# Kernel tuning notes

Measured on AMD Instinct MI355X. Metric: run time of the kernel, lower is better.

Reference implementation:

```python
import jax, jax.numpy as jnp
import numpy as np

B = 4096
D1 = 2048   # APPEARANCE_DIM
D2 = 1024   # POSE_DIM
DF = 8192   # FUSED_DIM
LN_EPS = 1e-5
L2_EPS = 1e-12


def setup_inputs() -> dict:
    key = jax.random.key(0)
    ks = jax.random.split(key, 6)
    x = jax.random.normal(ks[0], (B, D1), dtype=jnp.float32)
    y = jax.random.normal(ks[1], (B, D2), dtype=jnp.float32)
    h1 = jax.random.randint(ks[2], (D1,), 0, DF, dtype=jnp.int32)
    h2 = jax.random.randint(ks[3], (D2,), 0, DF, dtype=jnp.int32)
    s1 = (2 * jax.random.randint(ks[4], (D1,), 0, 2) - 1).astype(jnp.float32)
    s2 = (2 * jax.random.randint(ks[5], (D2,), 0, 2) - 1).astype(jnp.float32)
    gamma = jnp.ones((DF,), dtype=jnp.float32)
    beta = jnp.zeros((DF,), dtype=jnp.float32)
    return {"x": x, "y": y, "s1": s1, "s2": s2, "gamma": gamma,
            "beta": beta, "h1": h1, "h2": h2}


def count_sketch(v, h, s, out_dim):
    # v: [B, Din], h: [Din] int indices into out_dim, s: [Din] +-1 signs
    # single vectorized scatter-add along the feature axis
    return jnp.zeros((v.shape[0], out_dim), v.dtype).at[:, h].add(v * s)


def reference(x, y, s1, s2, gamma, beta, h1, h2):
    x_sk = count_sketch(x, h1, s1, DF)          # [B, DF]
    y_sk = count_sketch(y, h2, s2, DF)          # [B, DF]
    # circular convolution via FFT
    fused = jnp.fft.ifft(jnp.fft.fft(x_sk, axis=1) * jnp.fft.fft(y_sk, axis=1),
                         axis=1).real           # [B, DF]
    # LayerNorm over last dim
    mu = jnp.mean(fused, axis=-1, keepdims=True)
    var = jnp.mean(jnp.square(fused - mu), axis=-1, keepdims=True)
    normed = (fused - mu) * jax.lax.rsqrt(var + LN_EPS) * gamma + beta
    # F.normalize(p=2, dim=1)
    nrm = jnp.linalg.norm(normed, axis=1, keepdims=True)
    return normed / jnp.maximum(nrm, L2_EPS)
```

## Files before the change

### kernel.cpp

```cpp
#include <hip/hip_runtime.h>
#include <math.h>

#define DF 8192
#define NT 1024

#define SW(i) ((i) ^ ((((i) >> 4) & 7) << 2))

__device__ __forceinline__ float2 cmul(float2 a, float2 b) {
    return make_float2(a.x * b.x - a.y * b.y, a.x * b.y + a.y * b.x);
}
__device__ __forceinline__ float2 cadd(float2 a, float2 b) { return make_float2(a.x + b.x, a.y + b.y); }
__device__ __forceinline__ float2 csub(float2 a, float2 b) { return make_float2(a.x - b.x, a.y - b.y); }
__device__ __forceinline__ float2 cmuli(float2 a)  { return make_float2(-a.y, a.x); }
__device__ __forceinline__ float2 cmulmi(float2 a) { return make_float2(a.y, -a.x); }

#define RT_H 0.70710678118654752f

__device__ __forceinline__ int brev10(int x) { return (int)(__brev((unsigned)x) >> 22); }

__device__ __forceinline__ void bf_dif(float2& a, float2& b, float2 W) {
    float2 d = csub(a, b);
    a = cadd(a, b);
    b = cmul(d, W);
}
__device__ __forceinline__ void bf_dit(float2& a, float2& b, float2 W) {
    float2 bw = cmul(b, W);
    float2 ta = a;
    a = cadd(ta, bw);
    b = csub(ta, bw);
}
__device__ __forceinline__ void bf_dit1(float2& a, float2& b) {
    float2 tb = b, ta = a;
    a = cadd(ta, tb);
    b = csub(ta, tb);
}
__device__ __forceinline__ void bf_diti(float2& a, float2& b) {
    float2 bw = cmuli(b);
    float2 ta = a;
    a = cadd(ta, bw);
    b = csub(ta, bw);
}

__device__ __forceinline__ void fft8_dif(float2 v[8], float2 w) {
    const float2 w2 = cmul(w, w);
    const float2 w4 = cmul(w2, w2);
    bf_dif(v[0], v[4], w);
    bf_dif(v[1], v[5], cmul(w, make_float2(RT_H, -RT_H)));
    bf_dif(v[2], v[6], cmulmi(w));
    bf_dif(v[3], v[7], cmul(w, make_float2(-RT_H, -RT_H)));
    bf_dif(v[0], v[2], w2);
    bf_dif(v[1], v[3], cmulmi(w2));
    bf_dif(v[4], v[6], w2);
    bf_dif(v[5], v[7], cmulmi(w2));
    bf_dif(v[0], v[1], w4);
    bf_dif(v[2], v[3], w4);
    bf_dif(v[4], v[5], w4);
    bf_dif(v[6], v[7], w4);
}

__device__ __forceinline__ void fft4_dit(float2 v[4], float2 q) {
    const float2 q2 = cmul(q, q);
    bf_dit(v[0], v[1], q2);
    bf_dit(v[2], v[3], q2);
    bf_dit(v[0], v[2], q);
    bf_dit(v[1], v[3], cmuli(q));
}

__device__ __forceinline__ float2 mega_combine(float2 A, float2 B, float2 PA, float2 PB,
                                               float2 W, float invN) {
    float X1r = 0.5f * (A.x + PB.x), X1i = 0.5f * (A.y - PB.y);
    float Y1r = 0.5f * (A.y + PB.y), Y1i = 0.5f * (PB.x - A.x);
    float2 P1 = make_float2((X1r * Y1r - X1i * Y1i) * invN, (X1r * Y1i + X1i * Y1r) * invN);
    float X2r = 0.5f * (B.x + PA.x), X2i = 0.5f * (B.y - PA.y);
    float Y2r = 0.5f * (B.y + PA.y), Y2i = 0.5f * (PA.x - B.x);
    float2 P2 = make_float2((X2r * Y2r - X2i * Y2i) * invN, (X2r * Y2i + X2i * Y2r) * invN);
    float2 S = cadd(P1, P2);
    float2 D = csub(P1, P2);
    float2 Dw = cmul(D, W);
    return make_float2(S.x - Dw.y, S.y + Dw.x);
}

__global__ __launch_bounds__(NT, 8)
void mcb5(const float* __restrict__ x, const float* __restrict__ y,
          const float* __restrict__ s1, const float* __restrict__ s2,
          const float* __restrict__ gamma, const float* __restrict__ beta,
          const int* __restrict__ h1, const int* __restrict__ h2,
          float* __restrict__ out)
{
    __shared__ float2 z[DF];
    const int t = threadIdx.x;
    const int row = blockIdx.x;

    {
        float4* z4 = (float4*)z;
        #pragma unroll
        for (int m = 0; m < 4; ++m) z4[t + NT * m] = make_float4(0.f, 0.f, 0.f, 0.f);
    }
    __syncthreads();

    {
        float2 xv = ((const float2*)(x + (size_t)row * 2048))[t];
        float2 sv = ((const float2*)s1)[t];
        int2   hv = ((const int2*)h1)[t];
        atomicAdd(&z[SW(hv.x)].x, xv.x * sv.x);
        atomicAdd(&z[SW(hv.y)].x, xv.y * sv.y);
        float yv = (y + (size_t)row * 1024)[t];
        atomicAdd(&z[SW(h2[t])].y, yv * s2[t]);
    }
    __syncthreads();

    float sn, cs;

    {
        float2 v[8];
        #pragma unroll
        for (int m = 0; m < 8; ++m) v[m] = z[SW(t + 1024 * m)];
        __sincosf(-(float)M_PI / 4096.f * (float)t, &sn, &cs);
        fft8_dif(v, make_float2(cs, sn));
        #pragma unroll
        for (int m = 0; m < 8; ++m) z[SW(t + 1024 * m)] = v[m];
    }
    __syncthreads();

    {
        const int lo = t & 127, hi = t >> 7;
        float2 v[8];
        #pragma unroll
        for (int m = 0; m < 8; ++m) v[m] = z[SW(lo + 128 * m + 1024 * hi)];
        __sincosf(-(float)M_PI / 512.f * (float)lo, &sn, &cs);
        fft8_dif(v, make_float2(cs, sn));
        #pragma unroll
        for (int m = 0; m < 8; ++m) z[SW(lo + 128 * m + 1024 * hi)] = v[m];
    }
    __syncthreads();

    {
        const int lo = t & 15, hi = t >> 4;
        float2 v[8];
        #pragma unroll
        for (int m = 0; m < 8; ++m) v[m] = z[SW(lo + 16 * m + 128 * hi)];
        __sincosf(-(float)M_PI / 64.f * (float)lo, &sn, &cs);
        fft8_dif(v, make_float2(cs, sn));
        #pragma unroll
        for (int m = 0; m < 8; ++m) z[SW(lo + 16 * m + 128 * hi)] = v[m];
    }
    __syncthreads();

    {
        const int lo = t & 1, hi = t >> 1;
        float2 v[8];
        #pragma unroll
        for (int m = 0; m < 8; ++m) v[m] = z[SW(lo + 2 * m + 16 * hi)];
        __sincosf(-(float)M_PI / 8.f * (float)lo, &sn, &cs);
        fft8_dif(v, make_float2(cs, sn));
        #pragma unroll
        for (int m = 0; m < 8; ++m) z[SW(lo + 2 * m + 16 * hi)] = v[m];
    }
    __syncthreads();

    float2 u[4];
    {
        const int R  = brev10(t);
        const int tp = (R == 0) ? 0 : brev10(1024 - R);
        __sincosf((float)M_PI / 4096.f * (float)R, &sn, &cs);
        const float2 wR = make_float2(cs, sn);
        const float invN = 1.f / 8192.f;
        const float2 rc[4] = { make_float2(1.f, 0.f),  make_float2(0.f, 1.f),
                               make_float2(RT_H, RT_H), make_float2(-RT_H, RT_H) };
        const int TBL[4] = {0, 1, 3, 2};
        #pragma unroll
        for (int g = 0; g < 4; ++g) {
            int pg = (t == 0) ? TBL[g] : (3 - g);
            float4 q = *(const float4*)&z[SW(8 * t + 2 * g)];
            float4 r = *(const float4*)&z[SW(8 * tp + 2 * pg)];
            float2 A  = make_float2(q.x + q.z, q.y + q.w);
            float2 B  = make_float2(q.x - q.z, q.y - q.w);
            float2 PA = make_float2(r.x + r.z, r.y + r.w);
            float2 PB = make_float2(r.x - r.z, r.y - r.w);
            if (t == 0 && g == 0) { float2 sw = PA; PA = PB; PB = sw; }
            u[g] = mega_combine(A, B, PA, PB, cmul(wR, rc[g]), invN);
        }
        bf_dit1(u[0], u[1]);
        bf_dit1(u[2], u[3]);
        bf_dit1(u[0], u[2]);
        bf_diti(u[1], u[3]);
    }
    __syncthreads();
    *(float4*)&z[SW(4 * t)]     = make_float4(u[0].x, u[0].y, u[1].x, u[1].y);
    *(float4*)&z[SW(4 * t + 2)] = make_float4(u[2].x, u[2].y, u[3].x, u[3].y);
    __syncthreads();

    {
        const int lo = t & 3, hi = t >> 2;
        #pragma unroll
        for (int m = 0; m < 4; ++m) u[m] = z[SW(lo + 4 * m + 16 * hi)];
        __sincosf((float)M_PI / 8.f * (float)lo, &sn, &cs);
        fft4_dit(u, make_float2(cs, sn));
        #pragma unroll
        for (int m = 0; m < 4; ++m) z[SW(lo + 4 * m + 16 * hi)] = u[m];
    }
    __syncthreads();

    {
        const int lo = t & 15, hi = t >> 4;
        #pragma unroll
        for (int m = 0; m < 4; ++m) u[m] = z[SW(lo + 16 * m + 64 * hi)];
        __sincosf((float)M_PI / 32.f * (float)lo, &sn, &cs);
        fft4_dit(u, make_float2(cs, sn));
        #pragma unroll
        for (int m = 0; m < 4; ++m) z[SW(lo + 16 * m + 64 * hi)] = u[m];
    }
    __syncthreads();

    {
        const int lo = t & 63, hi = t >> 6;
        #pragma unroll
        for (int m = 0; m < 4; ++m) u[m] = z[SW(lo + 64 * m + 256 * hi)];
        __sincosf((float)M_PI / 128.f * (float)lo, &sn, &cs);
        fft4_dit(u, make_float2(cs, sn));
        #pragma unroll
        for (int m = 0; m < 4; ++m) z[SW(lo + 64 * m + 256 * hi)] = u[m];
    }
    __syncthreads();

    {
        const int lo = t & 255, hi = t >> 8;
        #pragma unroll
        for (int m = 0; m < 4; ++m) u[m] = z[SW(lo + 256 * m + 1024 * hi)];
        __sincosf((float)M_PI / 512.f * (float)lo, &sn, &cs);
        fft4_dit(u, make_float2(cs, sn));
        #pragma unroll
        for (int m = 0; m < 4; ++m) z[SW(lo + 256 * m + 1024 * hi)] = u[m];
    }
    __syncthreads();

    #pragma unroll
    for (int m = 0; m < 4; ++m) u[m] = z[SW(t + 1024 * m)];
    __sincosf((float)M_PI / 2048.f * (float)t, &sn, &cs);
    fft4_dit(u, make_float2(cs, sn));

    float lsum = 0.f, lsq = 0.f;
    #pragma unroll
    for (int m = 0; m < 4; ++m) {
        lsum += u[m].x + u[m].y;
        lsq  += u[m].x * u[m].x + u[m].y * u[m].y;
    }
    #pragma unroll
    for (int k = 32; k >= 1; k >>= 1) { lsum += __shfl_xor(lsum, k); lsq += __shfl_xor(lsq, k); }
    const int wid = t >> 6, lane = t & 63;
    __syncthreads();
    if (lane == 0) z[wid] = make_float2(lsum, lsq);
    __syncthreads();
    float tsum = 0.f, tsq = 0.f;
    #pragma unroll
    for (int w = 0; w < 16; ++w) { tsum += z[w].x; tsq += z[w].y; }
    const float mu   = tsum * (1.f / (float)DF);
    const float var  = tsq * (1.f / (float)DF) - mu * mu;
    const float rstd = rsqrtf(var + 1e-5f);

    const float2* g2  = (const float2*)gamma;
    const float2* bt2 = (const float2*)beta;
    float lsq2 = 0.f;
    #pragma unroll
    for (int m = 0; m < 4; ++m) {
        int i = t + 1024 * m;
        float2 g = g2[i], bb = bt2[i];
        float ne = (u[m].x - mu) * rstd * g.x + bb.x;
        float no = (u[m].y - mu) * rstd * g.y + bb.y;
        u[m] = make_float2(ne, no);
        lsq2 += ne * ne + no * no;
    }
    #pragma unroll
    for (int k = 32; k >= 1; k >>= 1) lsq2 += __shfl_xor(lsq2, k);
    if (lane == 0) z[32 + wid].x = lsq2;
    __syncthreads();
    float t2 = 0.f;
    #pragma unroll
    for (int w = 0; w < 16; ++w) t2 += z[32 + w].x;
    const float inv = 1.f / fmaxf(sqrtf(t2), 1e-12f);

    float2* o2 = (float2*)(out + (size_t)row * DF);
    #pragma unroll
    for (int m = 0; m < 4; ++m)
        o2[t + 1024 * m] = make_float2(u[m].x * inv, u[m].y * inv);
}

extern "C" void kernel_launch(void* const* d_in, const int* in_sizes, int n_in,
                              void* d_out, int out_size, void* d_ws, size_t ws_size,
                              hipStream_t stream) {
    const float* x     = (const float*)d_in[0];
    const float* y     = (const float*)d_in[1];
    const float* s1    = (const float*)d_in[2];
    const float* s2    = (const float*)d_in[3];
    const float* gamma = (const float*)d_in[4];
    const float* beta  = (const float*)d_in[5];
    const int*   h1    = (const int*)d_in[6];
    const int*   h2    = (const int*)d_in[7];
    float* out = (float*)d_out;

    hipLaunchKernelGGL(mcb5, dim3(4096), dim3(NT), 0, stream,
                       x, y, s1, s2, gamma, beta, h1, h2, out);
}
```

Measured before the change: 190.9 us.

## Process two rows per block with packed float2 FFT lanes and wave-local syncs

Each block now handles two batch rows at once. Their x/y sketches are packed into float4 LDS entries so every FFT butterfly works on float2 vectors (rows A and B) and shares twiddle computation, index math and barriers across both rows. Block-wide barriers between stages whose data stays inside one wavefront are replaced with an lgkmcnt wait, and the swizzle is changed to suit 16-byte entries. The cost is twice the LDS per block (128 KB), lower occupancy bounds, and more registers per thread.

```diff
diff --git a/kernel.cpp b/kernel.cpp
--- a/kernel.cpp
+++ b/kernel.cpp
@@ -4,285 +4,308 @@
 #define DF 8192
 #define NT 1024
 
-#define SW(i) ((i) ^ ((((i) >> 4) & 7) << 2))
-
-__device__ __forceinline__ float2 cmul(float2 a, float2 b) {
-    return make_float2(a.x * b.x - a.y * b.y, a.x * b.y + a.y * b.x);
-}
-__device__ __forceinline__ float2 cadd(float2 a, float2 b) { return make_float2(a.x + b.x, a.y + b.y); }
-__device__ __forceinline__ float2 csub(float2 a, float2 b) { return make_float2(a.x - b.x, a.y - b.y); }
-__device__ __forceinline__ float2 cmuli(float2 a)  { return make_float2(-a.y, a.x); }
-__device__ __forceinline__ float2 cmulmi(float2 a) { return make_float2(a.y, -a.x); }
-
+#define SW4(i) ((i) ^ (((i) >> 3) & 7))
+
+#define WAVE_SYNC asm volatile("s_waitcnt lgkmcnt(0)" ::: "memory")
+
+typedef float cf2 __attribute__((ext_vector_type(2)));
+typedef float cf4 __attribute__((ext_vector_type(4)));
+
+#define RT_C 0.92387953251128674f
+#define RT_S 0.38268343236508977f
 #define RT_H 0.70710678118654752f
 
+struct sc { float re, im; };
+__device__ __forceinline__ sc smul(sc a, sc b) { return sc{a.re * b.re - a.im * b.im, a.re * b.im + a.im * b.re}; }
+__device__ __forceinline__ sc smi(sc a) { return sc{a.im, -a.re}; }
+__device__ __forceinline__ sc spi(sc a) { return sc{-a.im, a.re}; }
+
+__device__ __forceinline__ void pdif(cf2& ar, cf2& ai, cf2& br, cf2& bi, sc W) {
+    cf2 dr = ar - br, di = ai - bi;
+    ar += br; ai += bi;
+    br = dr * W.re - di * W.im;
+    bi = dr * W.im + di * W.re;
+}
+__device__ __forceinline__ void pdit(cf2& ar, cf2& ai, cf2& br, cf2& bi, sc W) {
+    cf2 wr = br * W.re - bi * W.im;
+    cf2 wi = br * W.im + bi * W.re;
+    br = ar - wr; bi = ai - wi;
+    ar += wr; ai += wi;
+}
+__device__ __forceinline__ void pdit1(cf2& ar, cf2& ai, cf2& br, cf2& bi) {
+    cf2 tr = br, ti = bi;
+    br = ar - tr; bi = ai - ti;
+    ar += tr; ai += ti;
+}
+__device__ __forceinline__ void pditi(cf2& ar, cf2& ai, cf2& br, cf2& bi) {
+    cf2 wr = -bi, wi = br;
+    br = ar - wr; bi = ai - wi;
+    ar += wr; ai += wi;
+}
+
+__device__ __forceinline__ void fft8_dif_p(cf2 vr[8], cf2 vi[8], sc w) {
+    sc w2 = smul(w, w), w4 = smul(w2, w2);
+    pdif(vr[0], vi[0], vr[4], vi[4], w);
+    pdif(vr[1], vi[1], vr[5], vi[5], smul(w, sc{RT_H, -RT_H}));
+    pdif(vr[2], vi[2], vr[6], vi[6], smi(w));
+    pdif(vr[3], vi[3], vr[7], vi[7], smul(w, sc{-RT_H, -RT_H}));
+    pdif(vr[0], vi[0], vr[2], vi[2], w2);
+    pdif(vr[1], vi[1], vr[3], vi[3], smi(w2));
+    pdif(vr[4], vi[4], vr[6], vi[6], w2);
+    pdif(vr[5], vi[5], vr[7], vi[7], smi(w2));
+    pdif(vr[0], vi[0], vr[1], vi[1], w4);
+    pdif(vr[2], vi[2], vr[3], vi[3], w4);
+    pdif(vr[4], vi[4], vr[5], vi[5], w4);
+    pdif(vr[6], vi[6], vr[7], vi[7], w4);
+}
+
+__device__ __forceinline__ void fft4_dit_p(cf2 ur[4], cf2 ui[4], sc q) {
+    sc q2 = smul(q, q);
+    pdit(ur[0], ui[0], ur[1], ui[1], q2);
+    pdit(ur[2], ui[2], ur[3], ui[3], q2);
+    pdit(ur[0], ui[0], ur[2], ui[2], q);
+    pdit(ur[1], ui[1], ur[3], ui[3], spi(q));
+}
+
 __device__ __forceinline__ int brev10(int x) { return (int)(__brev((unsigned)x) >> 22); }
 
-__device__ __forceinline__ void bf_dif(float2& a, float2& b, float2 W) {
-    float2 d = csub(a, b);
-    a = cadd(a, b);
-    b = cmul(d, W);
-}
-__device__ __forceinline__ void bf_dit(float2& a, float2& b, float2 W) {
-    float2 bw = cmul(b, W);
-    float2 ta = a;
-    a = cadd(ta, bw);
-    b = csub(ta, bw);
-}
-__device__ __forceinline__ void bf_dit1(float2& a, float2& b) {
-    float2 tb = b, ta = a;
-    a = cadd(ta, tb);
-    b = csub(ta, tb);
-}
-__device__ __forceinline__ void bf_diti(float2& a, float2& b) {
-    float2 bw = cmuli(b);
-    float2 ta = a;
-    a = cadd(ta, bw);
-    b = csub(ta, bw);
-}
-
-__device__ __forceinline__ void fft8_dif(float2 v[8], float2 w) {
-    const float2 w2 = cmul(w, w);
-    const float2 w4 = cmul(w2, w2);
-    bf_dif(v[0], v[4], w);
-    bf_dif(v[1], v[5], cmul(w, make_float2(RT_H, -RT_H)));
-    bf_dif(v[2], v[6], cmulmi(w));
-    bf_dif(v[3], v[7], cmul(w, make_float2(-RT_H, -RT_H)));
-    bf_dif(v[0], v[2], w2);
-    bf_dif(v[1], v[3], cmulmi(w2));
-    bf_dif(v[4], v[6], w2);
-    bf_dif(v[5], v[7], cmulmi(w2));
-    bf_dif(v[0], v[1], w4);
-    bf_dif(v[2], v[3], w4);
-    bf_dif(v[4], v[5], w4);
-    bf_dif(v[6], v[7], w4);
-}
-
-__device__ __forceinline__ void fft4_dit(float2 v[4], float2 q) {
-    const float2 q2 = cmul(q, q);
-    bf_dit(v[0], v[1], q2);
-    bf_dit(v[2], v[3], q2);
-    bf_dit(v[0], v[2], q);
-    bf_dit(v[1], v[3], cmuli(q));
-}
-
-__device__ __forceinline__ float2 mega_combine(float2 A, float2 B, float2 PA, float2 PB,
-                                               float2 W, float invN) {
-    float X1r = 0.5f * (A.x + PB.x), X1i = 0.5f * (A.y - PB.y);
-    float Y1r = 0.5f * (A.y + PB.y), Y1i = 0.5f * (PB.x - A.x);
-    float2 P1 = make_float2((X1r * Y1r - X1i * Y1i) * invN, (X1r * Y1i + X1i * Y1r) * invN);
-    float X2r = 0.5f * (B.x + PA.x), X2i = 0.5f * (B.y - PA.y);
-    float Y2r = 0.5f * (B.y + PA.y), Y2i = 0.5f * (PA.x - B.x);
-    float2 P2 = make_float2((X2r * Y2r - X2i * Y2i) * invN, (X2r * Y2i + X2i * Y2r) * invN);
-    float2 S = cadd(P1, P2);
-    float2 D = csub(P1, P2);
-    float2 Dw = cmul(D, W);
-    return make_float2(S.x - Dw.y, S.y + Dw.x);
-}
-
-__global__ __launch_bounds__(NT, 8)
-void mcb5(const float* __restrict__ x, const float* __restrict__ y,
+__device__ __forceinline__ cf2 shfl_xor_cf2(cf2 v, int mask) {
+    double d;
+    __builtin_memcpy(&d, &v, 8);
+    d = __shfl_xor(d, mask);
+    cf2 r;
+    __builtin_memcpy(&r, &d, 8);
+    return r;
+}
+
+__global__ __launch_bounds__(NT, 4)
+void mcb9(const float* __restrict__ x, const float* __restrict__ y,
           const float* __restrict__ s1, const float* __restrict__ s2,
           const float* __restrict__ gamma, const float* __restrict__ beta,
           const int* __restrict__ h1, const int* __restrict__ h2,
           float* __restrict__ out)
 {
-    __shared__ float2 z[DF];
-    const int t = threadIdx.x;
-    const int row = blockIdx.x;
-
-    {
-        float4* z4 = (float4*)z;
-        #pragma unroll
-        for (int m = 0; m < 4; ++m) z4[t + NT * m] = make_float4(0.f, 0.f, 0.f, 0.f);
-    }
-    __syncthreads();
-
-    {
-        float2 xv = ((const float2*)(x + (size_t)row * 2048))[t];
+    __shared__ cf4 z4[DF];
+    float* zf = (float*)z4;
+    const int t    = threadIdx.x;
+    const int lane = t & 63;
+    const int wv   = t >> 6;
+    const int rA = blockIdx.x * 2, rB = rA + 1;
+
+    #pragma unroll
+    for (int m = 0; m < 8; ++m) z4[t + NT * m] = cf4{0.f, 0.f, 0.f, 0.f};
+    __syncthreads();
+
+    {
+        float2 xa = ((const float2*)(x + (size_t)rA * 2048))[t];
+        float2 xb = ((const float2*)(x + (size_t)rB * 2048))[t];
         float2 sv = ((const float2*)s1)[t];
         int2   hv = ((const int2*)h1)[t];
-        atomicAdd(&z[SW(hv.x)].x, xv.x * sv.x);
-        atomicAdd(&z[SW(hv.y)].x, xv.y * sv.y);
-        float yv = (y + (size_t)row * 1024)[t];
-        atomicAdd(&z[SW(h2[t])].y, yv * s2[t]);
+        int p0 = SW4(hv.x), p1 = SW4(hv.y);
+        atomicAdd(zf + 4 * p0 + 0, xa.x * sv.x);
+        atomicAdd(zf + 4 * p0 + 1, xb.x * sv.x);
+        atomicAdd(zf + 4 * p1 + 0, xa.y * sv.y);
+        atomicAdd(zf + 4 * p1 + 1, xb.y * sv.y);
+        float ya = (y + (size_t)rA * 1024)[t];
+        float yb = (y + (size_t)rB * 1024)[t];
+        float tv = s2[t];
+        int q0 = SW4(h2[t]);
+        atomicAdd(zf + 4 * q0 + 2, ya * tv);
+        atomicAdd(zf + 4 * q0 + 3, yb * tv);
     }
     __syncthreads();
 
     float sn, cs;
-
-    {
-        float2 v[8];
-        #pragma unroll
-        for (int m = 0; m < 8; ++m) v[m] = z[SW(t + 1024 * m)];
-        __sincosf(-(float)M_PI / 4096.f * (float)t, &sn, &cs);
-        fft8_dif(v, make_float2(cs, sn));
-        #pragma unroll
-        for (int m = 0; m < 8; ++m) z[SW(t + 1024 * m)] = v[m];
-    }
+    cf2 vr[8], vi[8];
+
+    #pragma unroll
+    for (int m = 0; m < 8; ++m) { cf4 q = z4[SW4(t + 1024 * m)]; vr[m] = q.lo; vi[m] = q.hi; }
+    __sincosf(-(float)M_PI / 4096.f * (float)t, &sn, &cs);
+    fft8_dif_p(vr, vi, sc{cs, sn});
+    #pragma unroll
+    for (int m = 0; m < 8; ++m) { cf4 q; q.lo = vr[m]; q.hi = vi[m]; z4[SW4(t + 1024 * m)] = q; }
     __syncthreads();
 
     {
         const int lo = t & 127, hi = t >> 7;
-        float2 v[8];
-        #pragma unroll
-        for (int m = 0; m < 8; ++m) v[m] = z[SW(lo + 128 * m + 1024 * hi)];
+        #pragma unroll
+        for (int m = 0; m < 8; ++m) { cf4 q = z4[SW4(lo + 128 * m + 1024 * hi)]; vr[m] = q.lo; vi[m] = q.hi; }
         __sincosf(-(float)M_PI / 512.f * (float)lo, &sn, &cs);
-        fft8_dif(v, make_float2(cs, sn));
-        #pragma unroll
-        for (int m = 0; m < 8; ++m) z[SW(lo + 128 * m + 1024 * hi)] = v[m];
+        fft8_dif_p(vr, vi, sc{cs, sn});
+        #pragma unroll
+        for (int m = 0; m < 8; ++m) { cf4 q; q.lo = vr[m]; q.hi = vi[m]; z4[SW4(lo + 128 * m + 1024 * hi)] = q; }
     }
     __syncthreads();
 
     {
         const int lo = t & 15, hi = t >> 4;
-        float2 v[8];
-        #pragma unroll
-        for (int m = 0; m < 8; ++m) v[m] = z[SW(lo + 16 * m + 128 * hi)];
+        #pragma unroll
+        for (int m = 0; m < 8; ++m) { cf4 q = z4[SW4(lo + 16 * m + 128 * hi)]; vr[m] = q.lo; vi[m] = q.hi; }
         __sincosf(-(float)M_PI / 64.f * (float)lo, &sn, &cs);
-        fft8_dif(v, make_float2(cs, sn));
-        #pragma unroll
-        for (int m = 0; m < 8; ++m) z[SW(lo + 16 * m + 128 * hi)] = v[m];
-    }
-    __syncthreads();
+        fft8_dif_p(vr, vi, sc{cs, sn});
+        #pragma unroll
+        for (int m = 0; m < 8; ++m) { cf4 q; q.lo = vr[m]; q.hi = vi[m]; z4[SW4(lo + 16 * m + 128 * hi)] = q; }
+    }
+    WAVE_SYNC;
 
     {
         const int lo = t & 1, hi = t >> 1;
-        float2 v[8];
-        #pragma unroll
-        for (int m = 0; m < 8; ++m) v[m] = z[SW(lo + 2 * m + 16 * hi)];
-        __sincosf(-(float)M_PI / 8.f * (float)lo, &sn, &cs);
-        fft8_dif(v, make_float2(cs, sn));
-        #pragma unroll
-        for (int m = 0; m < 8; ++m) z[SW(lo + 2 * m + 16 * hi)] = v[m];
-    }
-    __syncthreads();
-
-    float2 u[4];
+        #pragma unroll
+        for (int m = 0; m < 8; ++m) { cf4 q = z4[SW4(lo + 2 * m + 16 * hi)]; vr[m] = q.lo; vi[m] = q.hi; }
+        sc w = lo ? sc{RT_C, -RT_S} : sc{1.f, 0.f};
+        fft8_dif_p(vr, vi, w);
+        #pragma unroll
+        for (int m = 0; m < 8; ++m) { cf4 q; q.lo = vr[m]; q.hi = vi[m]; z4[SW4(lo + 2 * m + 16 * hi)] = q; }
+    }
+    __syncthreads();
+
+    cf2 ur[4], ui[4];
     {
         const int R  = brev10(t);
         const int tp = (R == 0) ? 0 : brev10(1024 - R);
         __sincosf((float)M_PI / 4096.f * (float)R, &sn, &cs);
-        const float2 wR = make_float2(cs, sn);
-        const float invN = 1.f / 8192.f;
-        const float2 rc[4] = { make_float2(1.f, 0.f),  make_float2(0.f, 1.f),
-                               make_float2(RT_H, RT_H), make_float2(-RT_H, RT_H) };
+        const sc wR = sc{cs, sn};
+        const float q4 = 0.25f / 8192.f;
+        const sc rc[4] = { sc{1.f, 0.f}, sc{0.f, 1.f}, sc{RT_H, RT_H}, sc{-RT_H, RT_H} };
         const int TBL[4] = {0, 1, 3, 2};
         #pragma unroll
         for (int g = 0; g < 4; ++g) {
-            int pg = (t == 0) ? TBL[g] : (3 - g);
-            float4 q = *(const float4*)&z[SW(8 * t + 2 * g)];
-            float4 r = *(const float4*)&z[SW(8 * tp + 2 * pg)];
-            float2 A  = make_float2(q.x + q.z, q.y + q.w);
-            float2 B  = make_float2(q.x - q.z, q.y - q.w);
-            float2 PA = make_float2(r.x + r.z, r.y + r.w);
-            float2 PB = make_float2(r.x - r.z, r.y - r.w);
-            if (t == 0 && g == 0) { float2 sw = PA; PA = PB; PB = sw; }
-            u[g] = mega_combine(A, B, PA, PB, cmul(wR, rc[g]), invN);
+            cf4 e0 = z4[SW4(8 * t + 2 * g)];
+            cf4 e1 = z4[SW4(8 * t + 2 * g + 1)];
+            cf2 Ar = e0.lo + e1.lo, Ai = e0.hi + e1.hi;
+            cf2 Br = e0.lo - e1.lo, Bi = e0.hi - e1.hi;
+            int pb = (t == 0) ? (2 * TBL[g]) : (8 * tp + 2 * (3 - g));
+            cf4 r0 = z4[SW4(pb)];
+            cf4 r1 = z4[SW4(pb + 1)];
+            cf2 PAr = r0.lo + r1.lo, PAi = r0.hi + r1.hi;
+            cf2 PBr = r0.lo - r1.lo, PBi = r0.hi - r1.hi;
+            if (t == 0 && g == 0) {
+                cf2 s0 = PAr; PAr = PBr; PBr = s0;
+                cf2 s1_ = PAi; PAi = PBi; PBi = s1_;
+            }
+            cf2 T1r = Ar + PBr, T1i = Ai - PBi;
+            cf2 T2r = Ai + PBi, T2i = PBr - Ar;
+            cf2 P1r = (T1r * T2r - T1i * T2i) * q4;
+            cf2 P1i = (T1r * T2i + T1i * T2r) * q4;
+            cf2 U1r = Br + PAr, U1i = Bi - PAi;
+            cf2 U2r = Bi + PAi, U2i = PAr - Br;
+            cf2 P2r = (U1r * U2r - U1i * U2i) * q4;
+            cf2 P2i = (U1r * U2i + U1i * U2r) * q4;
+            sc W = smul(wR, rc[g]);
+            cf2 Sr = P1r + P2r, Si = P1i + P2i;
+            cf2 Dr = P1r - P2r, Di = P1i - P2i;
+            cf2 Dwr = Dr * W.re - Di * W.im;
+            cf2 Dwi = Dr * W.im + Di * W.re;
+            ur[g] = Sr - Dwi;
+            ui[g] = Si + Dwr;
         }
-        bf_dit1(u[0], u[1]);
-        bf_dit1(u[2], u[3]);
-        bf_dit1(u[0], u[2]);
-        bf_diti(u[1], u[3]);
-    }
-    __syncthreads();
-    *(float4*)&z[SW(4 * t)]     = make_float4(u[0].x, u[0].y, u[1].x, u[1].y);
-    *(float4*)&z[SW(4 * t + 2)] = make_float4(u[2].x, u[2].y, u[3].x, u[3].y);
-    __syncthreads();
+        pdit1(ur[0], ui[0], ur[1], ui[1]);
+        pdit1(ur[2], ui[2], ur[3], ui[3]);
+        pdit1(ur[0], ui[0], ur[2], ui[2]);
+        pditi(ur[1], ui[1], ur[3], ui[3]);
+    }
+    __syncthreads();
+    #pragma unroll
+    for (int c = 0; c < 4; ++c) { cf4 q; q.lo = ur[c]; q.hi = ui[c]; z4[SW4(4 * t + c)] = q; }
+    WAVE_SYNC;
 
     {
         const int lo = t & 3, hi = t >> 2;
         #pragma unroll
-        for (int m = 0; m < 4; ++m) u[m] = z[SW(lo + 4 * m + 16 * hi)];
+        for (int m = 0; m < 4; ++m) { cf4 q = z4[SW4(lo + 4 * m + 16 * hi)]; ur[m] = q.lo; ui[m] = q.hi; }
         __sincosf((float)M_PI / 8.f * (float)lo, &sn, &cs);
-        fft4_dit(u, make_float2(cs, sn));
-        #pragma unroll
-        for (int m = 0; m < 4; ++m) z[SW(lo + 4 * m + 16 * hi)] = u[m];
-    }
-    __syncthreads();
+        fft4_dit_p(ur, ui, sc{cs, sn});
+        #pragma unroll
+        for (int m = 0; m < 4; ++m) { cf4 q; q.lo = ur[m]; q.hi = ui[m]; z4[SW4(lo + 4 * m + 16 * hi)] = q; }
+    }
+    WAVE_SYNC;
 
     {
         const int lo = t & 15, hi = t >> 4;
         #pragma unroll
-        for (int m = 0; m < 4; ++m) u[m] = z[SW(lo + 16 * m + 64 * hi)];
+        for (int m = 0; m < 4; ++m) { cf4 q = z4[SW4(lo + 16 * m + 64 * hi)]; ur[m] = q.lo; ui[m] = q.hi; }
         __sincosf((float)M_PI / 32.f * (float)lo, &sn, &cs);
-        fft4_dit(u, make_float2(cs, sn));
-        #pragma unroll
-        for (int m = 0; m < 4; ++m) z[SW(lo + 16 * m + 64 * hi)] = u[m];
-    }
-    __syncthreads();
+        fft4_dit_p(ur, ui, sc{cs, sn});
+        #pragma unroll
+        for (int m = 0; m < 4; ++m) { cf4 q; q.lo = ur[m]; q.hi = ui[m]; z4[SW4(lo + 16 * m + 64 * hi)] = q; }
+    }
+    WAVE_SYNC;
 
     {
         const int lo = t & 63, hi = t >> 6;
         #pragma unroll
-        for (int m = 0; m < 4; ++m) u[m] = z[SW(lo + 64 * m + 256 * hi)];
+        for (int m = 0; m < 4; ++m) { cf4 q = z4[SW4(lo + 64 * m + 256 * hi)]; ur[m] = q.lo; ui[m] = q.hi; }
         __sincosf((float)M_PI / 128.f * (float)lo, &sn, &cs);
-        fft4_dit(u, make_float2(cs, sn));
-        #pragma unroll
-        for (int m = 0; m < 4; ++m) z[SW(lo + 64 * m + 256 * hi)] = u[m];
+        fft4_dit_p(ur, ui, sc{cs, sn});
+        #pragma unroll
+        for (int m = 0; m < 4; ++m) { cf4 q; q.lo = ur[m]; q.hi = ui[m]; z4[SW4(lo + 64 * m + 256 * hi)] = q; }
     }
     __syncthreads();
 
     {
         const int lo = t & 255, hi = t >> 8;
         #pragma unroll
-        for (int m = 0; m < 4; ++m) u[m] = z[SW(lo + 256 * m + 1024 * hi)];
+        for (int m = 0; m < 4; ++m) { cf4 q = z4[SW4(lo + 256 * m + 1024 * hi)]; ur[m] = q.lo; ui[m] = q.hi; }
         __sincosf((float)M_PI / 512.f * (float)lo, &sn, &cs);
-        fft4_dit(u, make_float2(cs, sn));
-        #pragma unroll
-        for (int m = 0; m < 4; ++m) z[SW(lo + 256 * m + 1024 * hi)] = u[m];
-    }
-    __syncthreads();
-
-    #pragma unroll
-    for (int m = 0; m < 4; ++m) u[m] = z[SW(t + 1024 * m)];
+        fft4_dit_p(ur, ui, sc{cs, sn});
+        #pragma unroll
+        for (int m = 0; m < 4; ++m) { cf4 q; q.lo = ur[m]; q.hi = ui[m]; z4[SW4(lo + 256 * m + 1024 * hi)] = q; }
+    }
+    __syncthreads();
+
+    #pragma unroll
+    for (int m = 0; m < 4; ++m) { cf4 q = z4[SW4(t + 1024 * m)]; ur[m] = q.lo; ui[m] = q.hi; }
     __sincosf((float)M_PI / 2048.f * (float)t, &sn, &cs);
-    fft4_dit(u, make_float2(cs, sn));
-
-    float lsum = 0.f, lsq = 0.f;
+    fft4_dit_p(ur, ui, sc{cs, sn});
+
+    cf2 ps = cf2{0.f, 0.f}, pq = cf2{0.f, 0.f};
     #pragma unroll
     for (int m = 0; m < 4; ++m) {
-        lsum += u[m].x + u[m].y;
-        lsq  += u[m].x * u[m].x + u[m].y * u[m].y;
-    }
-    #pragma unroll
-    for (int k = 32; k >= 1; k >>= 1) { lsum += __shfl_xor(lsum, k); lsq += __shfl_xor(lsq, k); }
-    const int wid = t >> 6, lane = t & 63;
-    __syncthreads();
-    if (lane == 0) z[wid] = make_float2(lsum, lsq);
-    __syncthreads();
-    float tsum = 0.f, tsq = 0.f;
-    #pragma unroll
-    for (int w = 0; w < 16; ++w) { tsum += z[w].x; tsq += z[w].y; }
-    const float mu   = tsum * (1.f / (float)DF);
-    const float var  = tsq * (1.f / (float)DF) - mu * mu;
-    const float rstd = rsqrtf(var + 1e-5f);
+        ps += ur[m] + ui[m];
+        pq += ur[m] * ur[m] + ui[m] * ui[m];
+    }
+    #pragma unroll
+    for (int k = 32; k >= 1; k >>= 1) { ps += shfl_xor_cf2(ps, k); pq += shfl_xor_cf2(pq, k); }
+    __syncthreads();
+    if (lane == 0) { cf4 q; q.lo = ps; q.hi = pq; z4[wv] = q; }
+    __syncthreads();
+    cf2 ts = cf2{0.f, 0.f}, tq = cf2{0.f, 0.f};
+    #pragma unroll
+    for (int w = 0; w < 16; ++w) { cf4 s = z4[w]; ts += s.lo; tq += s.hi; }
+    const cf2 mu2 = ts * (1.f / (float)DF);
+    const cf2 var2 = tq * (1.f / (float)DF) - mu2 * mu2;
+    const cf2 rstd2 = cf2{rsqrtf(var2.x + 1e-5f), rsqrtf(var2.y + 1e-5f)};
 
     const float2* g2  = (const float2*)gamma;
     const float2* bt2 = (const float2*)beta;
-    float lsq2 = 0.f;
+    cf2 pl = cf2{0.f, 0.f};
     #pragma unroll
     for (int m = 0; m < 4; ++m) {
         int i = t + 1024 * m;
         float2 g = g2[i], bb = bt2[i];
-        float ne = (u[m].x - mu) * rstd * g.x + bb.x;
-        float no = (u[m].y - mu) * rstd * g.y + bb.y;
-        u[m] = make_float2(ne, no);
-        lsq2 += ne * ne + no * no;
-    }
-    #pragma unroll
-    for (int k = 32; k >= 1; k >>= 1) lsq2 += __shfl_xor(lsq2, k);
-    if (lane == 0) z[32 + wid].x = lsq2;
-    __syncthreads();
-    float t2 = 0.f;
-    #pragma unroll
-    for (int w = 0; w < 16; ++w) t2 += z[32 + w].x;
-    const float inv = 1.f / fmaxf(sqrtf(t2), 1e-12f);
-
-    float2* o2 = (float2*)(out + (size_t)row * DF);
-    #pragma unroll
-    for (int m = 0; m < 4; ++m)
-        o2[t + 1024 * m] = make_float2(u[m].x * inv, u[m].y * inv);
+        cf2 nr = (ur[m] - mu2) * rstd2 * g.x + bb.x;
+        cf2 ni = (ui[m] - mu2) * rstd2 * g.y + bb.y;
+        ur[m] = nr; ui[m] = ni;
+        pl += nr * nr + ni * ni;
+    }
+    #pragma unroll
+    for (int k = 32; k >= 1; k >>= 1) pl += shfl_xor_cf2(pl, k);
+    if (lane == 0) { cf4 q; q.lo = pl; q.hi = cf2{0.f, 0.f}; z4[16 + wv] = q; }
+    __syncthreads();
+    cf2 tl = cf2{0.f, 0.f};
+    #pragma unroll
+    for (int w = 0; w < 16; ++w) tl += z4[16 + w].lo;
+    const float invA = 1.f / fmaxf(sqrtf(tl.x), 1e-12f);
+    const float invB = 1.f / fmaxf(sqrtf(tl.y), 1e-12f);
+
+    float2* oA = (float2*)(out + (size_t)rA * DF);
+    float2* oB = (float2*)(out + (size_t)rB * DF);
+    #pragma unroll
+    for (int m = 0; m < 4; ++m) {
+        int i = t + 1024 * m;
+        oA[i] = make_float2(ur[m].x * invA, ui[m].x * invA);
+        oB[i] = make_float2(ur[m].y * invB, ui[m].y * invB);
+    }
 }
 
 extern "C" void kernel_launch(void* const* d_in, const int* in_sizes, int n_in,
@@ -298,6 +321,6 @@
     const int*   h2    = (const int*)d_in[7];
     float* out = (float*)d_out;
 
-    hipLaunchKernelGGL(mcb5, dim3(4096), dim3(NT), 0, stream,
+    hipLaunchKernelGGL(mcb9, dim3(2048), dim3(NT), 0, stream,
                        x, y, s1, s2, gamma, beta, h1, h2, out);
 }
```

Result: no change. 188.2 us (-1.4%).
